# Performance work log

Hardware: AMD Instinct MI355X
Metric: run time of the kernel (lower is better)

Reference implementation:

```python
import math
import jax, jax.numpy as jnp
import numpy as np

B, L, D, I, S, DTR, K, PH = 8, 2048, 512, 256, 8, 32, 3, 128


def setup_inputs() -> dict:
    key = jax.random.key(0)
    ks = jax.random.split(key, 12)
    def nrm(k, shape, s=0.02):
        return jax.random.normal(k, shape, jnp.float32) * s
    # dt_proj bias: inverse-softplus of exp(linspace(log 0.02, log 0.2))
    dt_init = np.exp(np.linspace(math.log(0.02), math.log(0.2), I))
    dt_b = np.log(np.expm1(dt_init)).astype(np.float32)
    A_log = np.log(np.tile(np.arange(1, S + 1, dtype=np.float32), (I, 1)))
    return dict(
        x=jax.random.normal(ks[0], (B, L, D), jnp.float32),
        position=jax.random.uniform(ks[1], (B, L, 6), jnp.float32),
        ln_in_w=jnp.ones(D, jnp.float32), ln_in_b=jnp.zeros(D, jnp.float32),
        pos_w1=nrm(ks[2], (PH, 6), 0.1), pos_b1=jnp.zeros(PH, jnp.float32),
        pos_w2=nrm(ks[3], (D, PH), 0.05), pos_b2=jnp.zeros(D, jnp.float32),
        scan_in_w=nrm(ks[4], (2, D, D)),
        scan_cx_w=nrm(ks[5], (2, I, 1, K), 0.2),
        scan_cz_w=nrm(ks[6], (2, I, 1, K), 0.2),
        scan_xp_w=nrm(ks[7], (2, DTR + 2 * S, I)),
        scan_dt_w=nrm(ks[8], (2, I, DTR)),
        scan_dt_b=jnp.tile(jnp.asarray(dt_b)[None], (2, 1)),
        scan_Alog=jnp.tile(jnp.asarray(A_log)[None], (2, 1, 1)),
        scan_Dp=jnp.ones((2, I), jnp.float32),
        scan_out_w=nrm(ks[9], (2, D, D)),  # zero-init in source; randomized for non-trivial testing
        mix_w=nrm(ks[10], (D, 3 * D)),
        ln_out_w=jnp.ones(D, jnp.float32), ln_out_b=jnp.zeros(D, jnp.float32),
    )


def _ln(x, w, b, eps=1e-6):
    m = x.mean(-1, keepdims=True)
    v = ((x - m) ** 2).mean(-1, keepdims=True)
    return (x - m) * jax.lax.rsqrt(v + eps) * w + b


def _dwconv_silu(x, w):
    # x: [B, L, C], w: [C, 1, K] depthwise conv1d, 'same' padding, then SiLU
    y = jax.lax.conv_general_dilated(
        jnp.swapaxes(x, 1, 2), w, (1,), ((K // 2, K // 2),),
        feature_group_count=w.shape[0], dimension_numbers=('NCH', 'OIH', 'NCH'))
    return jax.nn.silu(jnp.swapaxes(y, 1, 2))


def _selective_scan(x, in_w, cx_w, cz_w, xp_w, dt_w, dt_b, Alog, Dp, out_w):
    # ReferenceSelectiveScan1D.forward, x: [B, L, D]
    xb, zb = jnp.split(x @ in_w.T, 2, axis=-1)
    xb = _dwconv_silu(xb, cx_w)
    zb = _dwconv_silu(zb, cz_w)
    proj = xb @ xp_w.T  # [B, L, DTR + 2S]
    dt_raw, b_raw, c_raw = jnp.split(proj, [DTR, DTR + S], axis=-1)
    delta = jnp.clip(jax.nn.softplus(dt_raw @ dt_w.T + dt_b), 1e-4, 1.0)  # [B, L, I]
    bt = jnp.tanh(b_raw)  # [B, L, S]
    ct = jnp.tanh(c_raw)  # [B, L, S]
    a = jax.nn.softplus(Alog) + 1e-4  # [I, S]
    xs = (jnp.swapaxes(delta, 0, 1), jnp.swapaxes(bt, 0, 1),
          jnp.swapaxes(ct, 0, 1), jnp.swapaxes(xb, 0, 1))

    def step(state, inp):
        d_t, b_t, c_t, x_t = inp
        decay = jnp.clip(jnp.exp(-d_t[..., None] * a), 1e-4, 1.0)  # [B, I, S]
        state = decay * state + (1.0 - decay) * (b_t[:, None, :] * x_t[..., None])
        y = jnp.einsum('bis,bs->bi', state, c_t) + Dp * x_t
        return state, y

    state0 = jnp.zeros((x.shape[0], I, S), jnp.float32)
    _, ys = jax.lax.scan(step, state0, xs)  # ys: [L, B, I]
    y = jnp.swapaxes(ys, 0, 1)
    return jnp.concatenate([y, zb], -1) @ out_w.T


def reference(x, position, ln_in_w, ln_in_b, pos_w1, pos_b1, pos_w2, pos_b2,
              scan_in_w, scan_cx_w, scan_cz_w, scan_xp_w, scan_dt_w, scan_dt_b,
              scan_Alog, scan_Dp, scan_out_w, mix_w, ln_out_w, ln_out_b):
    pos = jax.nn.gelu(position @ pos_w1.T + pos_b1, approximate=False) @ pos_w2.T + pos_b2
    si = _ln(x, ln_in_w, ln_in_b) + pos
    params = lambda i: (scan_in_w[i], scan_cx_w[i], scan_cz_w[i], scan_xp_w[i],
                        scan_dt_w[i], scan_dt_b[i], scan_Alog[i], scan_Dp[i], scan_out_w[i])
    fwd = _selective_scan(si, *params(0))
    bwd = jnp.flip(_selective_scan(jnp.flip(si, 1), *params(1)), 1)
    mixed = jnp.concatenate([fwd, bwd, si], -1) @ mix_w.T
    return _ln(mixed, ln_out_w, ln_out_b)
```

## Files before the change

kernel.cpp:

```cpp
#include <hip/hip_runtime.h>
#include <hip/hip_bf16.h>

typedef __hip_bfloat16 bf16;
typedef __attribute__((ext_vector_type(8))) short short8;
typedef __attribute__((ext_vector_type(4))) float floatx4;

#define BBB 8
#define LL 2048
#define DDD 512
#define II 256
#define SS 8
#define MM (BBB*LL)
#define CHUNK 32
#define NCH (LL/CHUNK)

#define WS_SI    0l
#define WS_U0    16777216l
#define WS_U1    33554432l
#define WS_XZ    50331648l
#define WS_POS   50331648l
#define WS_H     67108864l
#define WS_P     50331648l
#define WS_Q     58720256l
#define WS_SINB  67108864l
#define WS_XBC   83886080l
#define WS_MIXED 83886080l
#define WS_DELTA 100663296l
#define WS_BTCT  117440512l
#define WS_INWB  121634816l
#define WS_MIXWB 122683392l
#define WS_PW2B  124256256l
#define WS_OWT   124387328l
#define WS_WP    125435904l
#define WS_WD    126484480l
#define WS_XPWB  126746624l
#define WS_A2    126763008l
#define WS_WXT   126779392l
#define WS_WZT   126785536l

__device__ __forceinline__ float b2f(unsigned short u) {
    return __uint_as_float(((unsigned)u) << 16);
}
__device__ __forceinline__ float bload(const bf16* p) {
    return b2f(*(const unsigned short*)p);
}
__device__ __forceinline__ void bstore(bf16* p, float v) {
    *p = __float2bfloat16(v);
}
__device__ __forceinline__ float softplus_f(float x) {
    return fmaxf(x, 0.f) + log1pf(expf(-fabsf(x)));
}
__device__ __forceinline__ float silu_f(float x) {
    return x / (1.f + expf(-x));
}
__device__ __forceinline__ void gl_lds16(const bf16* g, void* l) {
    __builtin_amdgcn_global_load_lds(
        (const __attribute__((address_space(1))) unsigned int*)g,
        (__attribute__((address_space(3))) unsigned int*)l, 16, 0, 0);
}
__device__ __forceinline__ void block_mean_rstd(float v0, float v1, float* red,
                                                float& mean, float& rstd) {
    float s = v0 + v1, q = v0*v0 + v1*v1;
    #pragma unroll
    for (int off = 32; off > 0; off >>= 1) {
        s += __shfl_down(s, off);
        q += __shfl_down(q, off);
    }
    int w = threadIdx.x >> 6, lane = threadIdx.x & 63;
    if (lane == 0) { red[w*2] = s; red[w*2+1] = q; }
    __syncthreads();
    if (threadIdx.x == 0) {
        float ts = 0.f, tq = 0.f;
        #pragma unroll
        for (int i = 0; i < 4; ++i) { ts += red[i*2]; tq += red[i*2+1]; }
        red[8] = ts; red[9] = tq;
    }
    __syncthreads();
    float ts = red[8], tq = red[9];
    mean = ts * (1.f/DDD);
    float var = tq * (1.f/DDD) - mean*mean;
    rstd = rsqrtf(var + 1e-6f);
}

__global__ __launch_bounds__(256)
void k_prep(const float* __restrict__ position, const float* __restrict__ pw1,
            const float* __restrict__ pb1, bf16* __restrict__ H,
            const float* __restrict__ ow, bf16* __restrict__ owT,
            const float* __restrict__ mixw, bf16* __restrict__ mixwb,
            const float* __restrict__ inw, bf16* __restrict__ inwb,
            const float* __restrict__ dtw, const float* __restrict__ xpw,
            bf16* __restrict__ Wd,
            const float* __restrict__ posw2, bf16* __restrict__ pw2b,
            bf16* __restrict__ xpwb,
            const float* __restrict__ Alog, float* __restrict__ a2,
            const float* __restrict__ cxw, const float* __restrict__ czw,
            float* __restrict__ wxT, float* __restrict__ wzT) {
    int bb = blockIdx.x;
    int tid = threadIdx.x;
    if (bb < 8192) {
        long idx = (long)bb*256 + tid;
        long row = idx >> 7; int ph = idx & 127;
        const float* p = position + row*6;
        const float* w = pw1 + ph*6;
        float v = pb1[ph];
        #pragma unroll
        for (int j = 0; j < 6; ++j) v = fmaf(p[j], w[j], v);
        v = 0.5f * v * (1.f + erff(v * 0.70710678118654752440f));
        bstore(H + idx, v);
    } else if (bb < 10240) {
        long idx = (long)(bb - 8192)*256 + tid;
        long d = idx >> 18; long rem = idx & 262143;
        long k = rem >> 9, c = rem & 511;
        bstore(owT + idx, ow[d*262144 + c*512 + k]);
    } else if (bb < 11008) {
        int i = (bb - 10240)*256*4 + tid*4;
        float4 v = *(const float4*)(mixw + i);
        bf16 t[4] = {__float2bfloat16(v.x), __float2bfloat16(v.y),
                     __float2bfloat16(v.z), __float2bfloat16(v.w)};
        *(ushort4*)(mixwb + i) = *(ushort4*)t;
    } else if (bb < 11520) {
        int i = (bb - 11008)*256*4 + tid*4;
        float4 v = *(const float4*)(inw + i);
        bf16 t[4] = {__float2bfloat16(v.x), __float2bfloat16(v.y),
                     __float2bfloat16(v.z), __float2bfloat16(v.w)};
        *(ushort4*)(inwb + i) = *(ushort4*)t;
    } else if (bb < 12032) {
        int local = bb - 11520;
        int d = local >> 8, i = local & 255, j = tid;
        const float* wr = dtw + (long)d*II*32 + i*32;
        const float* xp = xpw + (long)d*48*II;
        float acc = 0.f;
        #pragma unroll
        for (int k = 0; k < 32; ++k) acc = fmaf(wr[k], xp[k*II + j], acc);
        bstore(Wd + ((long)d*II + i)*II + j, acc);
    } else if (bb < 12096) {
        int i = (bb - 12032)*256*4 + tid*4;
        float4 v = *(const float4*)(posw2 + i);
        bf16 t[4] = {__float2bfloat16(v.x), __float2bfloat16(v.y),
                     __float2bfloat16(v.z), __float2bfloat16(v.w)};
        *(ushort4*)(pw2b + i) = *(ushort4*)t;
    } else if (bb < 12128) {
        int idx = (bb - 12096)*256 + tid;
        int d = idx >> 12, rem = idx & 4095;
        bstore(xpwb + idx, xpw[(long)d*48*II + 32*II + rem]);
    } else if (bb < 12144) {
        int idx = (bb - 12128)*256 + tid;
        float a = softplus_f(Alog[idx]) + 1e-4f;
        a2[idx] = -1.4426950408889634f * a;
    } else {
        int idx = (bb - 12144)*256 + tid;
        if (idx < 1536) {
            int d = idx / 768, rem = idx % 768;
            int k = rem >> 8, i = rem & 255;
            int kk = d ? (2 - k) : k;
            wxT[idx] = cxw[d*768 + i*3 + kk];
            wzT[idx] = czw[d*768 + i*3 + kk];
        }
    }
}

__global__ __launch_bounds__(256) void k_ln_add(const float* __restrict__ x,
                                                const bf16* __restrict__ posout,
                                                const float* __restrict__ lnw,
                                                const float* __restrict__ lnb,
                                                const float* __restrict__ pb2,
                                                bf16* __restrict__ si) {
    __shared__ float red[10];
    long row = blockIdx.x; int t = threadIdx.x;
    float v0 = x[row*DDD + t], v1 = x[row*DDD + t + 256];
    float mean, rstd;
    block_mean_rstd(v0, v1, red, mean, rstd);
    float p0 = bload(posout + row*DDD + t)       + pb2[t];
    float p1 = bload(posout + row*DDD + t + 256) + pb2[t + 256];
    bstore(si + row*DDD + t,       (v0-mean)*rstd*lnw[t]     + lnb[t]     + p0);
    bstore(si + row*DDD + t + 256, (v1-mean)*rstd*lnw[t+256] + lnb[t+256] + p1);
}

#define GEMM_COMPUTE(Sa, Sb)                                                      \
    do {                                                                          \
        _Pragma("unroll")                                                         \
        for (int kk = 0; kk < 2; ++kk) {                                          \
            const int sa_ = ((kk*4 + lq) ^ (lr & 7)) * 16;                        \
            short8 af[4], bfr[4];                                                 \
            _Pragma("unroll")                                                     \
            for (int mi = 0; mi < 4; ++mi)                                        \
                af[mi] = *(const short8*)((const char*)&Sa[wm*64 + mi*16 + lr][0] + sa_); \
            _Pragma("unroll")                                                     \
            for (int ni = 0; ni < 4; ++ni)                                        \
                bfr[ni] = *(const short8*)((const char*)&Sb[wn*64 + ni*16 + lr][0] + sa_); \
            _Pragma("unroll")                                                     \
            for (int mi = 0; mi < 4; ++mi)                                        \
                _Pragma("unroll")                                                 \
                for (int ni = 0; ni < 4; ++ni)                                    \
                    acc[mi][ni] = __builtin_amdgcn_mfma_f32_16x16x32_bf16(        \
                        af[mi], bfr[ni], acc[mi][ni], 0, 0, 0);                   \
        }                                                                         \
    } while (0)

template<typename TC, int EPI = 0>
__global__ __launch_bounds__(256)
void gemm_mfma(const bf16* __restrict__ A, long lda,
               const bf16* __restrict__ B, long ldb,
               TC* __restrict__ C, long ldc, int Kdim,
               const float* __restrict__ bias,
               long zA, long zB, long zC, long zbias) {
    __shared__ short As0[128][64], Bs0[128][64];
    __shared__ short As1[128][64], Bs1[128][64];
    const int tid = threadIdx.x;
    const int lane = tid & 63;
    const int wave = tid >> 6;
    const int wm = wave >> 1, wn = wave & 1;
    const int lr = lane & 15, lq = lane >> 4;
    A += (long)blockIdx.z * zA;
    B += (long)blockIdx.z * zB;
    C += (long)blockIdx.z * zC;
    const float* bp = bias ? bias + (long)blockIdx.z * zbias : nullptr;
    int nwg = gridDim.x * gridDim.y;
    int bid = blockIdx.y * gridDim.x + blockIdx.x;
    int wg = (bid & 7) * (nwg >> 3) + (bid >> 3);
    const long m0 = (long)(wg / gridDim.x) * 128;
    const long n0 = (long)(wg % gridDim.x) * 128;

    const bf16* gA[4]; const bf16* gB[4]; int off16[4];
    #pragma unroll
    for (int q = 0; q < 4; ++q) {
        int ch = q*256 + tid;
        int r = ch >> 3;
        int g = (ch & 7) ^ (r & 7);
        gA[q] = A + (m0 + r)*lda + g*8;
        gB[q] = B + (n0 + r)*ldb + g*8;
        off16[q] = (q*256 + wave*64) * 16;
    }
#define STAGE_G(Sa, Sb, k0)                                   \
    do {                                                      \
        _Pragma("unroll")                                     \
        for (int q = 0; q < 4; ++q) {                         \
            gl_lds16(gA[q] + (k0), (char*)(Sa) + off16[q]);   \
            gl_lds16(gB[q] + (k0), (char*)(Sb) + off16[q]);   \
        }                                                     \
    } while (0)

    floatx4 acc[4][4];
    #pragma unroll
    for (int i = 0; i < 4; ++i)
        #pragma unroll
        for (int j = 0; j < 4; ++j)
            acc[i][j] = (floatx4){0.f, 0.f, 0.f, 0.f};

    const int NT = Kdim >> 6;
    STAGE_G(As0, Bs0, 0);
    __syncthreads();
    for (int t = 0; t < NT; t += 2) {
        STAGE_G(As1, Bs1, (long)(t + 1) << 6);
        GEMM_COMPUTE(As0, Bs0);
        __syncthreads();
        if (t + 2 < NT) STAGE_G(As0, Bs0, (long)(t + 2) << 6);
        GEMM_COMPUTE(As1, Bs1);
        __syncthreads();
    }
#undef STAGE_G
    #pragma unroll
    for (int mi = 0; mi < 4; ++mi)
        #pragma unroll
        for (int ni = 0; ni < 4; ++ni)
            #pragma unroll
            for (int r = 0; r < 4; ++r) {
                long row = m0 + wm*64 + mi*16 + lq*4 + r;
                long col = n0 + wn*64 + ni*16 + lr;
                float v = acc[mi][ni][r];
                if (EPI == 1)
                    v = fminf(fmaxf(softplus_f(v + bp[col]), 1e-4f), 1.0f);
                if constexpr (sizeof(TC) == 2) bstore((bf16*)C + row*ldc + col, v);
                else ((float*)C)[row*ldc + col] = v;
            }
}

__global__ __launch_bounds__(256) void k_btct(const bf16* __restrict__ xbc,
                                              const bf16* __restrict__ xpwb,
                                              float* __restrict__ btct) {
    int d = blockIdx.y;
    int wave = threadIdx.x >> 6, lane = threadIdx.x & 63;
    long r0 = (long)blockIdx.x*64 + wave*16;
    int lr = lane & 15, lq = lane >> 4;
    const bf16* xb = xbc  + (long)d*MM*II;
    const bf16* wp = xpwb + (long)d*16*II;
    floatx4 acc = (floatx4){0.f, 0.f, 0.f, 0.f};
    #pragma unroll
    for (int k0 = 0; k0 < II; k0 += 32) {
        short8 af = *(const short8*)(xb + (r0 + lr)*II + k0 + lq*8);
        short8 bf = *(const short8*)(wp + lr*II + k0 + lq*8);
        acc = __builtin_amdgcn_mfma_f32_16x16x32_bf16(af, bf, acc, 0, 0, 0);
    }
    #pragma unroll
    for (int r = 0; r < 4; ++r) {
        long row = r0 + lq*4 + r;
        btct[((long)d*MM + row)*16 + lr] = tanhf(acc[r]);
    }
}

__global__ __launch_bounds__(256) void k_conv(const bf16* __restrict__ xz,
                                              const float* __restrict__ wxT,
                                              const float* __restrict__ wzT,
                                              bf16* __restrict__ xbc,
                                              bf16* __restrict__ u0,
                                              bf16* __restrict__ u1) {
    int d = blockIdx.y;
    long idx = (long)blockIdx.x*256 + threadIdx.x;
    long rg = idx >> 5; int i = (int)(idx & 31) * 8;
    long row0 = rg << 2;
    int l0 = (int)(row0 & (LL-1));
    const float* wxp = wxT + d*768 + i;
    const float* wzp = wzT + d*768 + i;
    float wxr[3][8], wzr[3][8];
    #pragma unroll
    for (int k = 0; k < 3; ++k) {
        *(float4*)&wxr[k][0] = *(const float4*)(wxp + k*256);
        *(float4*)&wxr[k][4] = *(const float4*)(wxp + k*256 + 4);
        *(float4*)&wzr[k][0] = *(const float4*)(wzp + k*256);
        *(float4*)&wzr[k][4] = *(const float4*)(wzp + k*256 + 4);
    }
    const bf16* base = xz + row0*1024 + (long)d*512 + i;
    short8 X[6], Z[6];
    #pragma unroll
    for (int k = 0; k < 6; ++k) {
        int gl = l0 - 1 + k;
        bool ok = (gl >= 0) && (gl < LL);
        if (ok) {
            X[k] = *(const short8*)(base + (long)(k-1)*1024);
            Z[k] = *(const short8*)(base + (long)(k-1)*1024 + 256);
        } else {
            X[k] = (short8){0,0,0,0,0,0,0,0};
            Z[k] = (short8){0,0,0,0,0,0,0,0};
        }
    }
    bf16* u = d ? u1 : u0;
    #pragma unroll
    for (int r = 0; r < 4; ++r) {
        bf16 ox[8], oz[8];
        #pragma unroll
        for (int j = 0; j < 8; ++j) {
            float ax = 0.f, az = 0.f;
            #pragma unroll
            for (int k = 0; k < 3; ++k) {
                ax = fmaf(b2f((unsigned short)X[r+k][j]), wxr[k][j], ax);
                az = fmaf(b2f((unsigned short)Z[r+k][j]), wzr[k][j], az);
            }
            ox[j] = __float2bfloat16(silu_f(ax));
            oz[j] = __float2bfloat16(silu_f(az));
        }
        *(short8*)(xbc + (long)d*MM*II + (row0+r)*II + i) = *(short8*)ox;
        *(short8*)(u + (row0+r)*512 + 256 + i) = *(short8*)oz;
    }
}

__global__ __launch_bounds__(256)
void gemm_mix3(const bf16* __restrict__ A0, const bf16* __restrict__ A1,
               const bf16* __restrict__ A2,
               const bf16* __restrict__ B0, const bf16* __restrict__ B1,
               const bf16* __restrict__ B2, long ldb2,
               bf16* __restrict__ C) {
    __shared__ short As0[128][64], Bs0[128][64];
    __shared__ short As1[128][64], Bs1[128][64];
    const int tid = threadIdx.x;
    const int lane = tid & 63;
    const int wave = tid >> 6;
    const int wm = wave >> 1, wn = wave & 1;
    const int lr = lane & 15, lq = lane >> 4;
    int nwg = gridDim.x * gridDim.y;
    int bid = blockIdx.y * gridDim.x + blockIdx.x;
    int wg = (bid & 7) * (nwg >> 3) + (bid >> 3);
    const long m0 = (long)(wg / gridDim.x) * 128;
    const long n0 = (long)(wg % gridDim.x) * 128;

    long aoff[4], boffA[4], boffB[4]; int off16[4];
    #pragma unroll
    for (int q = 0; q < 4; ++q) {
        int ch = q*256 + tid;
        int r = ch >> 3;
        int g = (ch & 7) ^ (r & 7);
        aoff[q]  = (m0 + r)*512 + g*8;
        boffA[q] = (n0 + r)*512 + g*8;
        boffB[q] = (n0 + r)*ldb2 + g*8;
        off16[q] = (q*256 + wave*64) * 16;
    }
#define STAGE_M(Sa, Sb, t)                                                   \
    do {                                                                     \
        int seg_ = (t) >> 3;                                                 \
        long kc_ = ((long)(t) << 6) & 511;                                   \
        const bf16* Ap_ = (seg_ == 0) ? A0 : (seg_ == 1 ? A1 : A2);          \
        const bf16* Bp_ = (seg_ == 0) ? B0 : (seg_ == 1 ? B1 : B2);          \
        _Pragma("unroll")                                                    \
        for (int q = 0; q < 4; ++q) {                                        \
            gl_lds16(Ap_ + aoff[q] + kc_, (char*)(Sa) + off16[q]);           \
            gl_lds16(Bp_ + (seg_ < 2 ? boffA[q] : boffB[q]) + kc_,           \
                     (char*)(Sb) + off16[q]);                                \
        }                                                                    \
    } while (0)

    floatx4 acc[4][4];
    #pragma unroll
    for (int i = 0; i < 4; ++i)
        #pragma unroll
        for (int j = 0; j < 4; ++j)
            acc[i][j] = (floatx4){0.f, 0.f, 0.f, 0.f};

    STAGE_M(As0, Bs0, 0);
    __syncthreads();
    for (int t = 0; t < 24; t += 2) {
        STAGE_M(As1, Bs1, t + 1);
        GEMM_COMPUTE(As0, Bs0);
        __syncthreads();
        if (t + 2 < 24) STAGE_M(As0, Bs0, t + 2);
        GEMM_COMPUTE(As1, Bs1);
        __syncthreads();
    }
#undef STAGE_M
    #pragma unroll
    for (int mi = 0; mi < 4; ++mi)
        #pragma unroll
        for (int ni = 0; ni < 4; ++ni)
            #pragma unroll
            for (int r = 0; r < 4; ++r) {
                long row = m0 + wm*64 + mi*16 + lq*4 + r;
                long col = n0 + wn*64 + ni*16 + lr;
                bstore(C + row*512 + col, acc[mi][ni][r]);
            }
}

__global__ __launch_bounds__(256) void k_scan1(const bf16* __restrict__ delta,
                                               const float* __restrict__ btct,
                                               const bf16* __restrict__ xbc,
                                               const float* __restrict__ a2,
                                               float* __restrict__ P,
                                               float* __restrict__ Q) {
    __shared__ float bts[CHUNK][8];
    int z = blockIdx.y;
    int d = z >> 3, b = z & 7;
    int c = blockIdx.x;
    int i = threadIdx.x;
    {
        int tt = threadIdx.x >> 3, s = threadIdx.x & 7;
        int t = c*CHUNK + tt;
        long l = d ? (LL-1-t) : t;
        long row = (long)b*LL + l;
        bts[tt][s] = btct[(long)d*MM*16 + row*16 + s];
    }
    const float* ap = a2 + ((long)d*II + i)*8;
    float4 aA = *(const float4*)(ap);
    float4 aB = *(const float4*)(ap + 4);
    float a2r[8] = {aA.x, aA.y, aA.z, aA.w, aB.x, aB.y, aB.z, aB.w};
    __syncthreads();

    int t0 = c*CHUNK;
    long l0 = d ? (long)(LL-1-t0) : (long)t0;
    long row0 = (long)b*LL + l0;
    long step = (d ? -1l : 1l) * II;
    const bf16* pd = delta + (long)d*MM*II + row0*II + i;
    const bf16* px = xbc   + (long)d*MM*II + row0*II + i;

    float Pv[8], Qv[8];
    #pragma unroll
    for (int s = 0; s < 8; ++s) { Pv[s] = 1.f; Qv[s] = 0.f; }

    float dv = bload(pd), xv = bload(px);
    for (int tt = 0; tt < CHUNK; ++tt) {
        float dvn = 0.f, xvn = 0.f;
        if (tt + 1 < CHUNK) { dvn = bload(pd + step); xvn = bload(px + step); }
        pd += step; px += step;
        float4 b0 = *(const float4*)&bts[tt][0];
        float4 b1 = *(const float4*)&bts[tt][4];
        float btv[8] = {b0.x, b0.y, b0.z, b0.w, b1.x, b1.y, b1.z, b1.w};
        #pragma unroll
        for (int s = 0; s < 8; ++s) {
            float dec = __builtin_amdgcn_fmed3f(exp2f(dv*a2r[s]), 1e-4f, 1.0f);
            Pv[s] *= dec;
            Qv[s] = fmaf(dec, Qv[s], (1.f - dec)*btv[s]*xv);
        }
        dv = dvn; xv = xvn;
    }
    long o = ((long)z*NCH + c)*2048 + (long)i*8;
    *(floatx4*)(P + o)     = (floatx4){Pv[0], Pv[1], Pv[2], Pv[3]};
    *(floatx4*)(P + o + 4) = (floatx4){Pv[4], Pv[5], Pv[6], Pv[7]};
    *(floatx4*)(Q + o)     = (floatx4){Qv[0], Qv[1], Qv[2], Qv[3]};
    *(floatx4*)(Q + o + 4) = (floatx4){Qv[4], Qv[5], Qv[6], Qv[7]};
}

__global__ __launch_bounds__(256) void k_scan2(const float* __restrict__ P,
                                               const float* __restrict__ Q,
                                               float* __restrict__ sinb) {
    int d = blockIdx.y;
    long idx = (long)blockIdx.x*256 + threadIdx.x;
    int b = (int)(idx >> 11); int rem = (int)(idx & 2047);
    long base = ((long)(d*8 + b)*NCH)*2048 + rem;
    float st = 0.f;
    for (int c = 0; c < NCH; ++c) {
        long o = base + (long)c*2048;
        sinb[o] = st;
        st = fmaf(P[o], st, Q[o]);
    }
}

__global__ __launch_bounds__(256) void k_scan3(const bf16* __restrict__ delta,
                                               const float* __restrict__ btct,
                                               const bf16* __restrict__ xbc,
                                               const float* __restrict__ a2,
                                               const float* __restrict__ Dp,
                                               const float* __restrict__ sinb,
                                               bf16* __restrict__ u0,
                                               bf16* __restrict__ u1) {
    __shared__ float bcs[CHUNK][16];
    int z = blockIdx.y;
    int d = z >> 3, b = z & 7;
    int c = blockIdx.x;
    int i = threadIdx.x;
    {
        int tt = threadIdx.x >> 3, col = (threadIdx.x & 7)*2;
        int t = c*CHUNK + tt;
        long l = d ? (LL-1-t) : t;
        long row = (long)b*LL + l;
        *(float2*)&bcs[tt][col] =
            *(const float2*)(btct + (long)d*MM*16 + row*16 + col);
    }
    const float* ap = a2 + ((long)d*II + i)*8;
    float4 aA = *(const float4*)(ap);
    float4 aB = *(const float4*)(ap + 4);
    float a2r[8] = {aA.x, aA.y, aA.z, aA.w, aB.x, aB.y, aB.z, aB.w};
    float dpv = Dp[d*II + i];
    const float* sb = sinb + ((long)z*NCH + c)*2048 + (long)i*8;
    float4 s0 = *(const float4*)(sb);
    float4 s1 = *(const float4*)(sb + 4);
    float st[8] = {s0.x, s0.y, s0.z, s0.w, s1.x, s1.y, s1.z, s1.w};
    __syncthreads();

    int t0 = c*CHUNK;
    long l0 = d ? (long)(LL-1-t0) : (long)t0;
    long row0 = (long)b*LL + l0;
    long step = (d ? -1l : 1l) * II;
    long ustep = (d ? -1l : 1l) * 512;
    const bf16* pd = delta + (long)d*MM*II + row0*II + i;
    const bf16* px = xbc   + (long)d*MM*II + row0*II + i;
    bf16* pu = (d ? u1 : u0) + row0*512 + i;

    float dv = bload(pd), xv = bload(px);
    for (int tt = 0; tt < CHUNK; ++tt) {
        float dvn = 0.f, xvn = 0.f;
        if (tt + 1 < CHUNK) { dvn = bload(pd + step); xvn = bload(px + step); }
        pd += step; px += step;
        const float4* q4 = (const float4*)&bcs[tt][0];
        float4 b0 = q4[0], b1 = q4[1], c0 = q4[2], c1 = q4[3];
        float btv[8] = {b0.x, b0.y, b0.z, b0.w, b1.x, b1.y, b1.z, b1.w};
        float ctv[8] = {c0.x, c0.y, c0.z, c0.w, c1.x, c1.y, c1.z, c1.w};
        float pa = dpv * xv;
        #pragma unroll
        for (int s = 0; s < 8; ++s) {
            float dec = __builtin_amdgcn_fmed3f(exp2f(dv*a2r[s]), 1e-4f, 1.0f);
            st[s] = fmaf(dec, st[s], (1.f - dec)*btv[s]*xv);
            pa = fmaf(st[s], ctv[s], pa);
        }
        bstore(pu, pa);
        pu += ustep;
        dv = dvn; xv = xvn;
    }
}

__global__ __launch_bounds__(256) void k_ln_out(const bf16* __restrict__ mixed,
                                                const float* __restrict__ w,
                                                const float* __restrict__ b,
                                                float* __restrict__ out) {
    __shared__ float red[10];
    long row = blockIdx.x; int t = threadIdx.x;
    float v0 = bload(mixed + row*DDD + t), v1 = bload(mixed + row*DDD + t + 256);
    float mean, rstd;
    block_mean_rstd(v0, v1, red, mean, rstd);
    out[row*DDD + t]       = (v0-mean)*rstd*w[t]     + b[t];
    out[row*DDD + t + 256] = (v1-mean)*rstd*w[t+256] + b[t+256];
}

extern "C" void kernel_launch(void* const* d_in, const int* in_sizes, int n_in,
                              void* d_out, int out_size, void* d_ws, size_t ws_size,
                              hipStream_t stream) {
    const float* x        = (const float*)d_in[0];
    const float* position = (const float*)d_in[1];
    const float* ln_in_w  = (const float*)d_in[2];
    const float* ln_in_b  = (const float*)d_in[3];
    const float* pos_w1   = (const float*)d_in[4];
    const float* pos_b1   = (const float*)d_in[5];
    const float* pos_w2   = (const float*)d_in[6];
    const float* pos_b2   = (const float*)d_in[7];
    const float* in_w     = (const float*)d_in[8];
    const float* cx_w     = (const float*)d_in[9];
    const float* cz_w     = (const float*)d_in[10];
    const float* xp_w     = (const float*)d_in[11];
    const float* dt_w     = (const float*)d_in[12];
    const float* dt_b     = (const float*)d_in[13];
    const float* Alog     = (const float*)d_in[14];
    const float* Dp       = (const float*)d_in[15];
    const float* out_w    = (const float*)d_in[16];
    const float* mix_w    = (const float*)d_in[17];
    const float* ln_out_w = (const float*)d_in[18];
    const float* ln_out_b = (const float*)d_in[19];
    float* out = (float*)d_out;

    char* base = (char*)d_ws;
    bf16*  si     = (bf16*)(base + WS_SI);
    bf16*  u0     = (bf16*)(base + WS_U0);
    bf16*  u1     = (bf16*)(base + WS_U1);
    bf16*  xz     = (bf16*)(base + WS_XZ);
    bf16*  posout = (bf16*)(base + WS_POS);
    bf16*  H      = (bf16*)(base + WS_H);
    float* Pb     = (float*)(base + WS_P);
    float* Qb     = (float*)(base + WS_Q);
    float* sinb   = (float*)(base + WS_SINB);
    bf16*  xbc    = (bf16*)(base + WS_XBC);
    bf16*  delta  = (bf16*)(base + WS_DELTA);
    float* btct   = (float*)(base + WS_BTCT);
    bf16*  mixed  = (bf16*)(base + WS_MIXED);
    bf16*  in_wb  = (bf16*)(base + WS_INWB);
    bf16*  mix_wb = (bf16*)(base + WS_MIXWB);
    bf16*  pw2b   = (bf16*)(base + WS_PW2B);
    bf16*  owT    = (bf16*)(base + WS_OWT);
    bf16*  Wp     = (bf16*)(base + WS_WP);
    bf16*  Wd     = (bf16*)(base + WS_WD);
    bf16*  xpwb   = (bf16*)(base + WS_XPWB);
    float* a2     = (float*)(base + WS_A2);
    float* wxT    = (float*)(base + WS_WXT);
    float* wzT    = (float*)(base + WS_WZT);

    k_prep<<<12150, 256, 0, stream>>>(position, pos_w1, pos_b1, H,
                                      out_w, owT, mix_w, mix_wb, in_w, in_wb,
                                      dt_w, xp_w, Wd, pos_w2, pw2b, xpwb,
                                      Alog, a2, cx_w, cz_w, wxT, wzT);
    gemm_mfma<bf16><<<dim3(4, 4, 2), 256, 0, stream>>>(
        mix_wb, 1536, owT, 512, Wp, 512, 512, nullptr, 512, 262144, 262144, 0);
    gemm_mfma<bf16><<<dim3(4, MM/128), 256, 0, stream>>>(
        H, 128, pw2b, 128, posout, 512, 128, nullptr, 0, 0, 0, 0);
    k_ln_add<<<MM, 256, 0, stream>>>(x, posout, ln_in_w, ln_in_b, pos_b2, si);
    gemm_mfma<bf16><<<dim3(8, MM/128), 256, 0, stream>>>(
        si, 512, in_wb, 512, xz, 1024, 512, nullptr, 0, 0, 0, 0);
    k_conv<<<dim3(512, 2), 256, 0, stream>>>(xz, wxT, wzT, xbc, u0, u1);
    gemm_mfma<bf16, 1><<<dim3(2, MM/128, 2), 256, 0, stream>>>(
        xbc, 256, Wd, 256, delta, 256, 256, dt_b,
        (long)MM*II, 65536, (long)MM*II, 256);
    k_btct<<<dim3(MM/64, 2), 256, 0, stream>>>(xbc, xpwb, btct);
    k_scan1<<<dim3(NCH, 16), 256, 0, stream>>>(delta, btct, xbc, a2, Pb, Qb);
    k_scan2<<<dim3(64, 2), 256, 0, stream>>>(Pb, Qb, sinb);
    k_scan3<<<dim3(NCH, 16), 256, 0, stream>>>(delta, btct, xbc, a2, Dp,
                                               sinb, u0, u1);
    gemm_mix3<<<dim3(4, MM/128), 256, 0, stream>>>(u0, u1, si,
                                                   Wp, Wp + 262144, mix_wb + 1024, 1536,
                                                   mixed);
    k_ln_out<<<MM, 256, 0, stream>>>(mixed, ln_out_w, ln_out_b, out);
}
```

Measured before the change: 356.4 us.

## Fuse input layernorm into pos-MLP GEMM epilogue and double-buffer GEMM loads

Per-row mean and rstd of x are now computed in the prep kernel, and the layernorm-plus-bias addition moves into the epilogue of the position-MLP GEMM. This removes the separate k_ln_add kernel and the bf16 posout round trip. The GEMM main loops also prefetch two stages ahead, using explicit vmcnt waits and raw barriers in place of __syncthreads, so global loads overlap with MFMA compute. In exchange, the epilogue does uncoalesced fp32 reads of x per output element, and the hand-written waitcnt logic assumes a fixed count of outstanding loads per stage.

```diff
diff --git a/kernel.cpp b/kernel.cpp
--- a/kernel.cpp
+++ b/kernel.cpp
@@ -18,7 +18,6 @@
 #define WS_U0    16777216l
 #define WS_U1    33554432l
 #define WS_XZ    50331648l
-#define WS_POS   50331648l
 #define WS_H     67108864l
 #define WS_P     50331648l
 #define WS_Q     58720256l
@@ -37,6 +36,8 @@
 #define WS_A2    126763008l
 #define WS_WXT   126779392l
 #define WS_WZT   126785536l
+#define WS_MRS   126791680l
+#define WS_LNBP  126922752l
 
 __device__ __forceinline__ float b2f(unsigned short u) {
     return __uint_as_float(((unsigned)u) << 16);
@@ -58,6 +59,10 @@
         (const __attribute__((address_space(1))) unsigned int*)g,
         (__attribute__((address_space(3))) unsigned int*)l, 16, 0, 0);
 }
+#define VMWAIT8() asm volatile("s_waitcnt vmcnt(8)" ::: "memory")
+#define VMWAIT0() asm volatile("s_waitcnt vmcnt(0)" ::: "memory")
+#define XBAR()    __builtin_amdgcn_s_barrier()
+
 __device__ __forceinline__ void block_mean_rstd(float v0, float v1, float* red,
                                                 float& mean, float& rstd) {
     float s = v0 + v1, q = v0*v0 + v1*v1;
@@ -83,7 +88,10 @@
 }
 
 __global__ __launch_bounds__(256)
-void k_prep(const float* __restrict__ position, const float* __restrict__ pw1,
+void k_prep(const float* __restrict__ x, float* __restrict__ mrs,
+            const float* __restrict__ lnb, const float* __restrict__ pb2,
+            float* __restrict__ lnbp,
+            const float* __restrict__ position, const float* __restrict__ pw1,
             const float* __restrict__ pb1, bf16* __restrict__ H,
             const float* __restrict__ ow, bf16* __restrict__ owT,
             const float* __restrict__ mixw, bf16* __restrict__ mixwb,
@@ -95,10 +103,17 @@
             const float* __restrict__ Alog, float* __restrict__ a2,
             const float* __restrict__ cxw, const float* __restrict__ czw,
             float* __restrict__ wxT, float* __restrict__ wzT) {
+    __shared__ float red[10];
     int bb = blockIdx.x;
     int tid = threadIdx.x;
-    if (bb < 8192) {
-        long idx = (long)bb*256 + tid;
+    if (bb < 16384) {
+        long row = bb;
+        float v0 = x[row*DDD + tid], v1 = x[row*DDD + tid + 256];
+        float mean, rstd;
+        block_mean_rstd(v0, v1, red, mean, rstd);
+        if (tid == 0) { mrs[row*2] = mean; mrs[row*2+1] = rstd; }
+    } else if (bb < 24576) {
+        long idx = (long)(bb - 16384)*256 + tid;
         long row = idx >> 7; int ph = idx & 127;
         const float* p = position + row*6;
         const float* w = pw1 + ph*6;
@@ -107,25 +122,25 @@
         for (int j = 0; j < 6; ++j) v = fmaf(p[j], w[j], v);
         v = 0.5f * v * (1.f + erff(v * 0.70710678118654752440f));
         bstore(H + idx, v);
-    } else if (bb < 10240) {
-        long idx = (long)(bb - 8192)*256 + tid;
+    } else if (bb < 26624) {
+        long idx = (long)(bb - 24576)*256 + tid;
         long d = idx >> 18; long rem = idx & 262143;
         long k = rem >> 9, c = rem & 511;
         bstore(owT + idx, ow[d*262144 + c*512 + k]);
-    } else if (bb < 11008) {
-        int i = (bb - 10240)*256*4 + tid*4;
+    } else if (bb < 27392) {
+        int i = (bb - 26624)*256*4 + tid*4;
         float4 v = *(const float4*)(mixw + i);
         bf16 t[4] = {__float2bfloat16(v.x), __float2bfloat16(v.y),
                      __float2bfloat16(v.z), __float2bfloat16(v.w)};
         *(ushort4*)(mixwb + i) = *(ushort4*)t;
-    } else if (bb < 11520) {
-        int i = (bb - 11008)*256*4 + tid*4;
+    } else if (bb < 27904) {
+        int i = (bb - 27392)*256*4 + tid*4;
         float4 v = *(const float4*)(inw + i);
         bf16 t[4] = {__float2bfloat16(v.x), __float2bfloat16(v.y),
                      __float2bfloat16(v.z), __float2bfloat16(v.w)};
         *(ushort4*)(inwb + i) = *(ushort4*)t;
-    } else if (bb < 12032) {
-        int local = bb - 11520;
+    } else if (bb < 28416) {
+        int local = bb - 27904;
         int d = local >> 8, i = local & 255, j = tid;
         const float* wr = dtw + (long)d*II*32 + i*32;
         const float* xp = xpw + (long)d*48*II;
@@ -133,22 +148,22 @@
         #pragma unroll
         for (int k = 0; k < 32; ++k) acc = fmaf(wr[k], xp[k*II + j], acc);
         bstore(Wd + ((long)d*II + i)*II + j, acc);
-    } else if (bb < 12096) {
-        int i = (bb - 12032)*256*4 + tid*4;
+    } else if (bb < 28480) {
+        int i = (bb - 28416)*256*4 + tid*4;
         float4 v = *(const float4*)(posw2 + i);
         bf16 t[4] = {__float2bfloat16(v.x), __float2bfloat16(v.y),
                      __float2bfloat16(v.z), __float2bfloat16(v.w)};
         *(ushort4*)(pw2b + i) = *(ushort4*)t;
-    } else if (bb < 12128) {
-        int idx = (bb - 12096)*256 + tid;
+    } else if (bb < 28512) {
+        int idx = (bb - 28480)*256 + tid;
         int d = idx >> 12, rem = idx & 4095;
         bstore(xpwb + idx, xpw[(long)d*48*II + 32*II + rem]);
-    } else if (bb < 12144) {
-        int idx = (bb - 12128)*256 + tid;
+    } else if (bb < 28528) {
+        int idx = (bb - 28512)*256 + tid;
         float a = softplus_f(Alog[idx]) + 1e-4f;
         a2[idx] = -1.4426950408889634f * a;
-    } else {
-        int idx = (bb - 12144)*256 + tid;
+    } else if (bb < 28534) {
+        int idx = (bb - 28528)*256 + tid;
         if (idx < 1536) {
             int d = idx / 768, rem = idx % 768;
             int k = rem >> 8, i = rem & 255;
@@ -156,24 +171,10 @@
             wxT[idx] = cxw[d*768 + i*3 + kk];
             wzT[idx] = czw[d*768 + i*3 + kk];
         }
-    }
-}
-
-__global__ __launch_bounds__(256) void k_ln_add(const float* __restrict__ x,
-                                                const bf16* __restrict__ posout,
-                                                const float* __restrict__ lnw,
-                                                const float* __restrict__ lnb,
-                                                const float* __restrict__ pb2,
-                                                bf16* __restrict__ si) {
-    __shared__ float red[10];
-    long row = blockIdx.x; int t = threadIdx.x;
-    float v0 = x[row*DDD + t], v1 = x[row*DDD + t + 256];
-    float mean, rstd;
-    block_mean_rstd(v0, v1, red, mean, rstd);
-    float p0 = bload(posout + row*DDD + t)       + pb2[t];
-    float p1 = bload(posout + row*DDD + t + 256) + pb2[t + 256];
-    bstore(si + row*DDD + t,       (v0-mean)*rstd*lnw[t]     + lnb[t]     + p0);
-    bstore(si + row*DDD + t + 256, (v1-mean)*rstd*lnw[t+256] + lnb[t+256] + p1);
+    } else {
+        int idx = (bb - 28534)*256 + tid;
+        lnbp[idx] = lnb[idx] + pb2[idx];
+    }
 }
 
 #define GEMM_COMPUTE(Sa, Sb)                                                      \
@@ -203,7 +204,9 @@
                const bf16* __restrict__ B, long ldb,
                TC* __restrict__ C, long ldc, int Kdim,
                const float* __restrict__ bias,
-               long zA, long zB, long zC, long zbias) {
+               long zA, long zB, long zC, long zbias,
+               const float* __restrict__ xf, const float* __restrict__ mrs,
+               const float* __restrict__ lnw, const float* __restrict__ lnbp) {
     __shared__ short As0[128][64], Bs0[128][64];
     __shared__ short As1[128][64], Bs1[128][64];
     const int tid = threadIdx.x;
@@ -249,15 +252,22 @@
 
     const int NT = Kdim >> 6;
     STAGE_G(As0, Bs0, 0);
-    __syncthreads();
-    for (int t = 0; t < NT; t += 2) {
-        STAGE_G(As1, Bs1, (long)(t + 1) << 6);
+    STAGE_G(As1, Bs1, 64);
+    int t = 0;
+    for (; t + 2 < NT; t += 2) {
+        VMWAIT8(); XBAR();
         GEMM_COMPUTE(As0, Bs0);
-        __syncthreads();
-        if (t + 2 < NT) STAGE_G(As0, Bs0, (long)(t + 2) << 6);
+        XBAR();
+        STAGE_G(As0, Bs0, (long)(t + 2) << 6);
+        VMWAIT8(); XBAR();
         GEMM_COMPUTE(As1, Bs1);
-        __syncthreads();
-    }
+        XBAR();
+        STAGE_G(As1, Bs1, (long)(t + 3) << 6);
+    }
+    VMWAIT8(); XBAR();
+    GEMM_COMPUTE(As0, Bs0);
+    VMWAIT0(); XBAR();
+    GEMM_COMPUTE(As1, Bs1);
 #undef STAGE_G
     #pragma unroll
     for (int mi = 0; mi < 4; ++mi)
@@ -270,6 +280,10 @@
                 float v = acc[mi][ni][r];
                 if (EPI == 1)
                     v = fminf(fmaxf(softplus_f(v + bp[col]), 1e-4f), 1.0f);
+                if (EPI == 2) {
+                    float2 ms = *(const float2*)(mrs + row*2);
+                    v += (xf[row*512 + col] - ms.x)*ms.y*lnw[col] + lnbp[col];
+                }
                 if constexpr (sizeof(TC) == 2) bstore((bf16*)C + row*ldc + col, v);
                 else ((float*)C)[row*ldc + col] = v;
             }
@@ -405,15 +419,22 @@
             acc[i][j] = (floatx4){0.f, 0.f, 0.f, 0.f};
 
     STAGE_M(As0, Bs0, 0);
-    __syncthreads();
-    for (int t = 0; t < 24; t += 2) {
-        STAGE_M(As1, Bs1, t + 1);
+    STAGE_M(As1, Bs1, 1);
+    int t = 0;
+    for (; t + 2 < 24; t += 2) {
+        VMWAIT8(); XBAR();
         GEMM_COMPUTE(As0, Bs0);
-        __syncthreads();
-        if (t + 2 < 24) STAGE_M(As0, Bs0, t + 2);
+        XBAR();
+        STAGE_M(As0, Bs0, t + 2);
+        VMWAIT8(); XBAR();
         GEMM_COMPUTE(As1, Bs1);
-        __syncthreads();
-    }
+        XBAR();
+        STAGE_M(As1, Bs1, t + 3);
+    }
+    VMWAIT8(); XBAR();
+    GEMM_COMPUTE(As0, Bs0);
+    VMWAIT0(); XBAR();
+    GEMM_COMPUTE(As1, Bs1);
 #undef STAGE_M
     #pragma unroll
     for (int mi = 0; mi < 4; ++mi)
@@ -606,7 +627,6 @@
     bf16*  u0     = (bf16*)(base + WS_U0);
     bf16*  u1     = (bf16*)(base + WS_U1);
     bf16*  xz     = (bf16*)(base + WS_XZ);
-    bf16*  posout = (bf16*)(base + WS_POS);
     bf16*  H      = (bf16*)(base + WS_H);
     float* Pb     = (float*)(base + WS_P);
     float* Qb     = (float*)(base + WS_Q);
@@ -625,22 +645,28 @@
     float* a2     = (float*)(base + WS_A2);
     float* wxT    = (float*)(base + WS_WXT);
     float* wzT    = (float*)(base + WS_WZT);
-
-    k_prep<<<12150, 256, 0, stream>>>(position, pos_w1, pos_b1, H,
+    float* mrs    = (float*)(base + WS_MRS);
+    float* lnbp   = (float*)(base + WS_LNBP);
+
+    k_prep<<<28536, 256, 0, stream>>>(x, mrs, ln_in_b, pos_b2, lnbp,
+                                      position, pos_w1, pos_b1, H,
                                       out_w, owT, mix_w, mix_wb, in_w, in_wb,
                                       dt_w, xp_w, Wd, pos_w2, pw2b, xpwb,
                                       Alog, a2, cx_w, cz_w, wxT, wzT);
-    gemm_mfma<bf16><<<dim3(4, 4, 2), 256, 0, stream>>>(
-        mix_wb, 1536, owT, 512, Wp, 512, 512, nullptr, 512, 262144, 262144, 0);
-    gemm_mfma<bf16><<<dim3(4, MM/128), 256, 0, stream>>>(
-        H, 128, pw2b, 128, posout, 512, 128, nullptr, 0, 0, 0, 0);
-    k_ln_add<<<MM, 256, 0, stream>>>(x, posout, ln_in_w, ln_in_b, pos_b2, si);
-    gemm_mfma<bf16><<<dim3(8, MM/128), 256, 0, stream>>>(
-        si, 512, in_wb, 512, xz, 1024, 512, nullptr, 0, 0, 0, 0);
+    gemm_mfma<bf16, 0><<<dim3(4, 4, 2), 256, 0, stream>>>(
+        mix_wb, 1536, owT, 512, Wp, 512, 512, nullptr, 512, 262144, 262144, 0,
+        nullptr, nullptr, nullptr, nullptr);
+    gemm_mfma<bf16, 2><<<dim3(4, MM/128), 256, 0, stream>>>(
+        H, 128, pw2b, 128, si, 512, 128, nullptr, 0, 0, 0, 0,
+        x, mrs, ln_in_w, lnbp);
+    gemm_mfma<bf16, 0><<<dim3(8, MM/128), 256, 0, stream>>>(
+        si, 512, in_wb, 512, xz, 1024, 512, nullptr, 0, 0, 0, 0,
+        nullptr, nullptr, nullptr, nullptr);
     k_conv<<<dim3(512, 2), 256, 0, stream>>>(xz, wxT, wzT, xbc, u0, u1);
     gemm_mfma<bf16, 1><<<dim3(2, MM/128, 2), 256, 0, stream>>>(
         xbc, 256, Wd, 256, delta, 256, 256, dt_b,
-        (long)MM*II, 65536, (long)MM*II, 256);
+        (long)MM*II, 65536, (long)MM*II, 256,
+        nullptr, nullptr, nullptr, nullptr);
     k_btct<<<dim3(MM/64, 2), 256, 0, stream>>>(xbc, xpwb, btct);
     k_scan1<<<dim3(NCH, 16), 256, 0, stream>>>(delta, btct, xbc, a2, Pb, Qb);
     k_scan2<<<dim3(64, 2), 256, 0, stream>>>(Pb, Qb, sinb);
```

Result: no change. 350.5 us (-1.7%).
